# Performance work log

Hardware: AMD Instinct MI355X
Metric: run time of the kernel (lower is better)

The kernel has to match this reference:

```python
import jax, jax.numpy as jnp
import numpy as np

DIM = 256
HEADS = 8
DIM_FF = 1024
N = 4096
HEAD_DIM = DIM // HEADS
SCALE = HEAD_DIM ** -0.5


def layer_norm(x, gamma, beta, eps=1e-5):
    mu = jnp.mean(x, axis=-1, keepdims=True)
    var = jnp.var(x, axis=-1, keepdims=True)
    return (x - mu) * jax.lax.rsqrt(var + eps) * gamma + beta


def setup_inputs() -> dict:
    key = jax.random.key(0)
    ks = jax.random.split(key, 8)
    x = jax.random.normal(ks[0], (N, DIM), dtype=jnp.float32)
    adj = jax.random.randint(ks[1], (N, N), 0, 2, dtype=jnp.int32)
    adj = adj.at[jnp.arange(N), jnp.arange(N)].set(1)  # self-loops
    s = 1.0 / np.sqrt(DIM)
    w_qkv = jax.random.normal(ks[2], (DIM, 3 * DIM), dtype=jnp.float32) * s
    w_proj = jax.random.normal(ks[3], (DIM, DIM), dtype=jnp.float32) * s
    b_proj = jnp.zeros((DIM,), jnp.float32)
    w1 = jax.random.normal(ks[4], (DIM, DIM_FF), dtype=jnp.float32) * s
    b1 = jnp.zeros((DIM_FF,), jnp.float32)
    w2 = jax.random.normal(ks[5], (DIM_FF, DIM), dtype=jnp.float32) / np.sqrt(DIM_FF)
    b2 = jnp.zeros((DIM,), jnp.float32)
    g1 = jnp.ones((DIM,), jnp.float32)
    be1 = jnp.zeros((DIM,), jnp.float32)
    g2 = jnp.ones((DIM,), jnp.float32)
    be2 = jnp.zeros((DIM,), jnp.float32)
    return {"x": x, "adj": adj, "w_qkv": w_qkv, "w_proj": w_proj,
            "b_proj": b_proj, "w1": w1, "b1": b1, "w2": w2, "b2": b2,
            "g1": g1, "be1": be1, "g2": g2, "be2": be2}


def reference(x, adj, w_qkv, w_proj, b_proj, w1, b1, w2, b2, g1, be1, g2, be2):
    n = x.shape[0]
    qkv = layer_norm(x, g1, be1) @ w_qkv            # (N, 3*dim)
    qkv = qkv.reshape(n, 3, HEADS, HEAD_DIM)
    q, k, v = qkv[:, 0], qkv[:, 1], qkv[:, 2]       # (N, h, d)
    scores = jnp.einsum('nhd,mhd->hnm', q, k) * SCALE
    mask = (adj != 0)[None, :, :]                    # (1, N, N)
    scores = jnp.where(mask, scores, -jnp.inf)
    attn = jax.nn.softmax(scores, axis=-1)           # (h, N, N)
    out = jnp.einsum('hnm,mhd->nhd', attn, v).reshape(n, DIM)
    x = x + out @ w_proj + b_proj
    h2 = layer_norm(x, g2, be2)
    ff = jax.nn.gelu(h2 @ w1 + b1) @ w2 + b2
    return x + ff
```

## Files before the change

kernel.cpp:

```cpp
#include <hip/hip_runtime.h>
#include <hip/hip_bf16.h>

#define NT 4096
#define DM 256
#define NH 8
#define HD 32
#define DFF 1024

typedef __attribute__((ext_vector_type(8))) short s8v;
typedef __attribute__((ext_vector_type(4))) float f4v;
typedef __attribute__((ext_vector_type(2))) float f2v;
typedef __attribute__((ext_vector_type(16))) float f16v;
typedef __attribute__((ext_vector_type(4))) int i4v;

static __device__ __forceinline__ unsigned short f2b(float f){
  union{float f; unsigned u;} v; v.f=f;
  return (unsigned short)((v.u + 0x7FFFu + ((v.u>>16)&1u))>>16);
}

static __device__ __forceinline__ void gl_lds16(const void* g, void* l){
  __builtin_amdgcn_global_load_lds(
      (const __attribute__((address_space(1))) unsigned int*)g,
      (__attribute__((address_space(3))) unsigned int*)l, 16, 0, 0);
}

__global__ __launch_bounds__(256) void prologue_kernel(
    const int* __restrict__ adj, unsigned long long* __restrict__ mask,
    const float* __restrict__ wqkv, const float* __restrict__ wproj,
    const float* __restrict__ w1, const float* __restrict__ w2,
    unsigned short* __restrict__ wqkvT, unsigned short* __restrict__ wprojT,
    unsigned short* __restrict__ w1T, unsigned short* __restrict__ w2T,
    const float* __restrict__ x, const float* __restrict__ g1,
    const float* __restrict__ be1, unsigned short* __restrict__ h1){
  int bx = blockIdx.x;
  if (bx < 1024){
    int wv = threadIdx.x>>6, lane = threadIdx.x&63;
    int base = (bx*4 + wv)*64;
    for (int it=0; it<16; ++it){
      int w0 = base + it*4;
      unsigned long long b0 = __ballot(adj[(long)(w0+0)*64 + lane]!=0);
      unsigned long long b1 = __ballot(adj[(long)(w0+1)*64 + lane]!=0);
      unsigned long long b2 = __ballot(adj[(long)(w0+2)*64 + lane]!=0);
      unsigned long long b3 = __ballot(adj[(long)(w0+3)*64 + lane]!=0);
      if (lane==0){ mask[w0]=b0; mask[w0+1]=b1; mask[w0+2]=b2; mask[w0+3]=b3; }
    }
  } else if (bx < 1152){
    int t = (bx-1024)*256 + threadIdx.x;
    const int stride = 128*256;
    for (int i=t;i<768*DM;i+=stride){int n=i>>8,k=i&255; wqkvT[i]=f2b(wqkv[k*768+n]);}
    for (int i=t;i<DM*DM;i+=stride){int n=i>>8,k=i&255; wprojT[i]=f2b(wproj[k*DM+n]);}
    for (int i=t;i<DFF*DM;i+=stride){int n=i>>8,k=i&255; w1T[i]=f2b(w1[k*DFF+n]);}
    for (int i=t;i<DM*DFF;i+=stride){int n=i/DFF,k=i-n*DFF; w2T[i]=f2b(w2[k*DM+n]);}
  } else {
    int wv = threadIdx.x>>6, lane = threadIdx.x&63;
    int rbase = (bx-1152)*4 + wv;
    for (int j=0;j<8;j++){
      int row = rbase + j*512;
      float4 v = *(const float4*)(x + row*DM + lane*4);
      float s = v.x+v.y+v.z+v.w;
      float sq = v.x*v.x+v.y*v.y+v.z*v.z+v.w*v.w;
      #pragma unroll
      for (int m=1;m<64;m<<=1){ s += __shfl_xor(s,m); sq += __shfl_xor(sq,m); }
      float mu = s*(1.0f/DM);
      float rs = rsqrtf(sq*(1.0f/DM) - mu*mu + 1e-5f);
      float4 gv = *(const float4*)(g1 + lane*4);
      float4 bv = *(const float4*)(be1 + lane*4);
      ushort4 o;
      o.x = f2b((v.x-mu)*rs*gv.x + bv.x);
      o.y = f2b((v.y-mu)*rs*gv.y + bv.y);
      o.z = f2b((v.z-mu)*rs*gv.z + bv.z);
      o.w = f2b((v.w-mu)*rs*gv.w + bv.w);
      *(ushort4*)(h1 + row*DM + lane*4) = o;
    }
  }
}

template<int KD, int MODE>
__global__ __launch_bounds__(256,4) void gemm24(const unsigned short* __restrict__ A,
            const unsigned short* __restrict__ Wt, const float* __restrict__ bias,
            void* __restrict__ outp,
            unsigned short* __restrict__ Qp, unsigned short* __restrict__ Kp,
            unsigned short* __restrict__ Vt){
  int wv = threadIdx.x>>6, lane = threadIdx.x&63;
  int lo = lane&15, hi = lane>>4;
  int r0 = blockIdx.y*32;
  int cbase = blockIdx.x*256 + wv*16;
  const unsigned short* ar0 = A + (r0+lo)*KD + hi*8;
  const unsigned short* ar1 = ar0 + 16*KD;
  const unsigned short* br0 = Wt + (cbase     +lo)*KD + hi*8;
  const unsigned short* br1 = Wt + (cbase+ 64 +lo)*KD + hi*8;
  const unsigned short* br2 = Wt + (cbase+128 +lo)*KD + hi*8;
  const unsigned short* br3 = Wt + (cbase+192 +lo)*KD + hi*8;
  f4v c00={0,0,0,0},c01={0,0,0,0},c02={0,0,0,0},c03={0,0,0,0};
  f4v c10={0,0,0,0},c11={0,0,0,0},c12={0,0,0,0},c13={0,0,0,0};
  #pragma unroll 2
  for (int k0=0;k0<KD;k0+=32){
    s8v a0 = *(const s8v*)(ar0 + k0);
    s8v a1 = *(const s8v*)(ar1 + k0);
    s8v b0 = *(const s8v*)(br0 + k0);
    s8v b1 = *(const s8v*)(br1 + k0);
    s8v b2 = *(const s8v*)(br2 + k0);
    s8v b3 = *(const s8v*)(br3 + k0);
    c00 = __builtin_amdgcn_mfma_f32_16x16x32_bf16(a0,b0,c00,0,0,0);
    c10 = __builtin_amdgcn_mfma_f32_16x16x32_bf16(a1,b0,c10,0,0,0);
    c01 = __builtin_amdgcn_mfma_f32_16x16x32_bf16(a0,b1,c01,0,0,0);
    c11 = __builtin_amdgcn_mfma_f32_16x16x32_bf16(a1,b1,c11,0,0,0);
    c02 = __builtin_amdgcn_mfma_f32_16x16x32_bf16(a0,b2,c02,0,0,0);
    c12 = __builtin_amdgcn_mfma_f32_16x16x32_bf16(a1,b2,c12,0,0,0);
    c03 = __builtin_amdgcn_mfma_f32_16x16x32_bf16(a0,b3,c03,0,0,0);
    c13 = __builtin_amdgcn_mfma_f32_16x16x32_bf16(a1,b3,c13,0,0,0);
  }
  const float scl2 = (float)(0.17677669529663687 * 1.4426950408889634);
  #pragma unroll
  for (int rt=0;rt<2;rt++){
    f4v e0 = rt? c10:c00, e1 = rt? c11:c01, e2 = rt? c12:c02, e3 = rt? c13:c03;
    int nb = r0 + rt*16 + hi*4;
    #pragma unroll
    for (int jj=0;jj<4;jj++){
      f4v acc = jj==0?e0 : jj==1?e1 : jj==2?e2 : e3;
      int c = cbase + jj*64 + lo;
      if (MODE==0){
        int which = c>>8, hd = c&255, hh = hd>>5, d = hd&31;
        #pragma unroll
        for (int r=0;r<4;r++){
          int n = nb + r;
          float val = acc[r];
          if (which==0) Qp[(hh*NT+n)*HD+d]=f2b(val*scl2);
          else if (which==1) Kp[(hh*NT+n)*HD+d]=f2b(val);
          else Vt[(hh*HD+d)*NT+n]=f2b(val);
        }
      }
    }
  }
}

__global__ __launch_bounds__(512,2) void attn_kernel(
    const unsigned short* __restrict__ Q, const unsigned short* __restrict__ K,
    const unsigned short* __restrict__ Vt, const unsigned* __restrict__ mb32,
    unsigned short* __restrict__ out){
  __shared__ float Opart[8][32][34];
  __shared__ float llS[8][32];
  int wv = threadIdx.x>>6, lane = threadIdx.x&63;
  int l31 = lane&31, hi5 = lane>>5;
  int h = blockIdx.x, q0 = blockIdx.y*64;
  const unsigned short* QbA = Q + (h*NT + q0 + l31)*HD + hi5*8;
  const unsigned short* QbB = QbA + 32*HD;
  s8v bqA1 = *(const s8v*)(QbA);
  s8v bqA2 = *(const s8v*)(QbA + 16);
  s8v bqB1 = *(const s8v*)(QbB);
  s8v bqB2 = *(const s8v*)(QbB + 16);
  const unsigned short* Kb = K + h*NT*HD;
  const unsigned short* Vb = Vt + (h*HD + l31)*NT;
  const unsigned* mrowA = mb32 + (q0+l31)*(NT/32) + wv*16;
  const unsigned* mrowB = mrowA + 32*(NT/32);
  const float C0 = -11.541560327111707f;
  const f16v c0v = {C0,C0,C0,C0,C0,C0,C0,C0,C0,C0,C0,C0,C0,C0,C0,C0};
  f2v lacA = {0.f,0.f}, lacB = {0.f,0.f};
  f16v accA = {0,0,0,0,0,0,0,0,0,0,0,0,0,0,0,0};
  f16v accB = {0,0,0,0,0,0,0,0,0,0,0,0,0,0,0,0};
  union SU { f16v v; f2v p[8]; };
  const unsigned short* Kt0 = Kb + (wv*512 + l31)*HD + hi5*8;
  s8v kc1 = *(const s8v*)(Kt0);
  s8v kc2 = *(const s8v*)(Kt0 + 16);
  for (int tg=0; tg<4; tg++){
    i4v mw4A = *(const i4v*)(mrowA + tg*4);
    i4v mw4B = *(const i4v*)(mrowB + tg*4);
    #pragma unroll
    for (int ti=0; ti<4; ti++){
      int t = tg*4 + ti;
      int m0 = wv*512 + t*32;
      const unsigned short* Vtp = Vb + m0 + hi5*8;
      s8v av1 = *(const s8v*)(Vtp);
      s8v av2 = *(const s8v*)(Vtp + 16);
      int tn = (t<15)? t+1 : 15;
      const unsigned short* Ktn = Kb + (wv*512 + tn*32 + l31)*HD + hi5*8;
      s8v kn1 = *(const s8v*)(Ktn);
      s8v kn2 = *(const s8v*)(Ktn + 16);
      SU sa, sb;
      __builtin_amdgcn_s_setprio(1);
      sa.v = __builtin_amdgcn_mfma_f32_32x32x16_bf16(kc1, bqA1, c0v, 0,0,0);
      sa.v = __builtin_amdgcn_mfma_f32_32x32x16_bf16(kc2, bqA2, sa.v, 0,0,0);
      sb.v = __builtin_amdgcn_mfma_f32_32x32x16_bf16(kc1, bqB1, c0v, 0,0,0);
      sb.v = __builtin_amdgcn_mfma_f32_32x32x16_bf16(kc2, bqB2, sb.v, 0,0,0);
      __builtin_amdgcn_s_setprio(0);
      unsigned mwA = ((unsigned)mw4A[ti]) >> (4*hi5);
      unsigned mwB = ((unsigned)mw4B[ti]) >> (4*hi5);
      #pragma unroll
      for (int r=0;r<16;r++){
        int bp = (r&3)+8*(r>>2);
        float pa = __builtin_amdgcn_exp2f(sa.v[r]);
        float pb = __builtin_amdgcn_exp2f(sb.v[r]);
        sa.v[r] = ((mwA >> bp) & 1u) ? pa : 0.0f;
        sb.v[r] = ((mwB >> bp) & 1u) ? pb : 0.0f;
      }
      #pragma unroll
      for (int i=0;i<8;i++){ lacA += sa.p[i]; lacB += sb.p[i]; }
      unsigned a0,a1,a2,a3,a4,a5,a6,a7, b0,b1,b2,b3,b4,b5,b6,b7;
      asm("v_cvt_pk_bf16_f32 %0, %1, %2" : "=v"(a0) : "v"(sa.v[0]),  "v"(sa.v[1]));
      asm("v_cvt_pk_bf16_f32 %0, %1, %2" : "=v"(a1) : "v"(sa.v[2]),  "v"(sa.v[3]));
      asm("v_cvt_pk_bf16_f32 %0, %1, %2" : "=v"(a2) : "v"(sa.v[4]),  "v"(sa.v[5]));
      asm("v_cvt_pk_bf16_f32 %0, %1, %2" : "=v"(a3) : "v"(sa.v[6]),  "v"(sa.v[7]));
      asm("v_cvt_pk_bf16_f32 %0, %1, %2" : "=v"(a4) : "v"(sa.v[8]),  "v"(sa.v[9]));
      asm("v_cvt_pk_bf16_f32 %0, %1, %2" : "=v"(a5) : "v"(sa.v[10]), "v"(sa.v[11]));
      asm("v_cvt_pk_bf16_f32 %0, %1, %2" : "=v"(a6) : "v"(sa.v[12]), "v"(sa.v[13]));
      asm("v_cvt_pk_bf16_f32 %0, %1, %2" : "=v"(a7) : "v"(sa.v[14]), "v"(sa.v[15]));
      asm("v_permlane32_swap_b32 %0, %1" : "+v"(a0), "+v"(a2));
      asm("v_permlane32_swap_b32 %0, %1" : "+v"(a1), "+v"(a3));
      asm("v_permlane32_swap_b32 %0, %1" : "+v"(a4), "+v"(a6));
      asm("v_permlane32_swap_b32 %0, %1" : "+v"(a5), "+v"(a7));
      asm("v_cvt_pk_bf16_f32 %0, %1, %2" : "=v"(b0) : "v"(sb.v[0]),  "v"(sb.v[1]));
      asm("v_cvt_pk_bf16_f32 %0, %1, %2" : "=v"(b1) : "v"(sb.v[2]),  "v"(sb.v[3]));
      asm("v_cvt_pk_bf16_f32 %0, %1, %2" : "=v"(b2) : "v"(sb.v[4]),  "v"(sb.v[5]));
      asm("v_cvt_pk_bf16_f32 %0, %1, %2" : "=v"(b3) : "v"(sb.v[6]),  "v"(sb.v[7]));
      asm("v_cvt_pk_bf16_f32 %0, %1, %2" : "=v"(b4) : "v"(sb.v[8]),  "v"(sb.v[9]));
      asm("v_cvt_pk_bf16_f32 %0, %1, %2" : "=v"(b5) : "v"(sb.v[10]), "v"(sb.v[11]));
      asm("v_cvt_pk_bf16_f32 %0, %1, %2" : "=v"(b6) : "v"(sb.v[12]), "v"(sb.v[13]));
      asm("v_cvt_pk_bf16_f32 %0, %1, %2" : "=v"(b7) : "v"(sb.v[14]), "v"(sb.v[15]));
      asm("v_permlane32_swap_b32 %0, %1" : "+v"(b0), "+v"(b2));
      asm("v_permlane32_swap_b32 %0, %1" : "+v"(b1), "+v"(b3));
      asm("v_permlane32_swap_b32 %0, %1" : "+v"(b4), "+v"(b6));
      asm("v_permlane32_swap_b32 %0, %1" : "+v"(b5), "+v"(b7));
      i4v pA1i = {(int)a0,(int)a1,(int)a2,(int)a3};
      i4v pA2i = {(int)a4,(int)a5,(int)a6,(int)a7};
      i4v pB1i = {(int)b0,(int)b1,(int)b2,(int)b3};
      i4v pB2i = {(int)b4,(int)b5,(int)b6,(int)b7};
      s8v pA1 = __builtin_bit_cast(s8v, pA1i);
      s8v pA2 = __builtin_bit_cast(s8v, pA2i);
      s8v pB1 = __builtin_bit_cast(s8v, pB1i);
      s8v pB2 = __builtin_bit_cast(s8v, pB2i);
      __builtin_amdgcn_s_setprio(1);
      accA = __builtin_amdgcn_mfma_f32_32x32x16_bf16(av1, pA1, accA, 0,0,0);
      accA = __builtin_amdgcn_mfma_f32_32x32x16_bf16(av2, pA2, accA, 0,0,0);
      accB = __builtin_amdgcn_mfma_f32_32x32x16_bf16(av1, pB1, accB, 0,0,0);
      accB = __builtin_amdgcn_mfma_f32_32x32x16_bf16(av2, pB2, accB, 0,0,0);
      __builtin_amdgcn_s_setprio(0);
      kc1 = kn1; kc2 = kn2;
    }
  }
  int tid = threadIdx.x;
  int qq = tid>>4, dd = 2*(tid&15);
  #pragma unroll
  for (int i=0;i<8;i++){
    int d = (2*i&3) + 8*(i>>1) + 4*hi5;
    float2 p2; p2.x = accA[2*i]; p2.y = accA[2*i+1];
    *(float2*)&Opart[wv][l31][d] = p2;
  }
  float lsumA = lacA[0] + lacA[1];
  lsumA += __shfl_xor(lsumA, 32);
  if (hi5==0) llS[wv][l31] = lsumA;
  __syncthreads();
  {
    float L=0.f, o0=0.f, o1=0.f;
    #pragma unroll
    for (int u=0;u<8;u++){
      L  += llS[u][qq];
      o0 += Opart[u][qq][dd];
      o1 += Opart[u][qq][dd+1];
    }
    float inv = 1.0f/L;
    float r0 = o0*inv, r1 = o1*inv;
    unsigned pw;
    asm("v_cvt_pk_bf16_f32 %0, %1, %2" : "=v"(pw) : "v"(r0), "v"(r1));
    *(unsigned*)(out + (q0+qq)*DM + h*HD + dd) = pw;
  }
  __syncthreads();
  #pragma unroll
  for (int i=0;i<8;i++){
    int d = (2*i&3) + 8*(i>>1) + 4*hi5;
    float2 p2; p2.x = accB[2*i]; p2.y = accB[2*i+1];
    *(float2*)&Opart[wv][l31][d] = p2;
  }
  float lsumB = lacB[0] + lacB[1];
  lsumB += __shfl_xor(lsumB, 32);
  if (hi5==0) llS[wv][l31] = lsumB;
  __syncthreads();
  {
    float L=0.f, o0=0.f, o1=0.f;
    #pragma unroll
    for (int u=0;u<8;u++){
      L  += llS[u][qq];
      o0 += Opart[u][qq][dd];
      o1 += Opart[u][qq][dd+1];
    }
    float inv = 1.0f/L;
    float r0 = o0*inv, r1 = o1*inv;
    unsigned pw;
    asm("v_cvt_pk_bf16_f32 %0, %1, %2" : "=v"(pw) : "v"(r0), "v"(r1));
    *(unsigned*)(out + (q0+32+qq)*DM + h*HD + dd) = pw;
  }
}

__global__ __launch_bounds__(512,2) void tail_kernel(
    const unsigned short* __restrict__ ao, const unsigned short* __restrict__ wprojT,
    const float* __restrict__ bproj, const float* __restrict__ x,
    const float* __restrict__ g2, const float* __restrict__ be2,
    const unsigned short* __restrict__ w1T, const float* __restrict__ b1,
    const unsigned short* __restrict__ w2T, const float* __restrict__ b2,
    float* __restrict__ outp){
  __shared__ unsigned short h2L[16][DM];
  __shared__ unsigned short gL[16][DFF];
  __shared__ float Ss[8][16], Sq[8][16];
  __shared__ __align__(16) unsigned char w2S[2][32768];
  int wv = threadIdx.x>>6, lane = threadIdx.x&63;
  int lo = lane&15, hi = lane>>4;
  int tid = threadIdx.x;
  int r0 = blockIdx.x*16;
  float t[2][4];

#define STAGE_W2(KT, BUF)                                                     \
  { _Pragma("unroll")                                                         \
    for (int rr=0; rr<4; ++rr){                                               \
      int col_ = rr*64 + (tid>>3);                                            \
      int ko_  = (tid&7) ^ (col_&7);                                          \
      gl_lds16(w2T + col_*DFF + (KT)*64 + ko_*8,                              \
               &w2S[BUF][rr*8192 + tid*16]);                                  \
    } }

  {
    const unsigned short* ar  = ao + (r0+lo)*DM + hi*8;
    const unsigned short* pb0 = wprojT + (wv*16     +lo)*DM + hi*8;
    const unsigned short* pb1 = wprojT + (wv*16+128 +lo)*DM + hi*8;
    f4v a0={0,0,0,0}, a1={0,0,0,0};
    #pragma unroll
    for (int k0=0;k0<DM;k0+=32){
      s8v a = *(const s8v*)(ar + k0);
      a0 = __builtin_amdgcn_mfma_f32_16x16x32_bf16(a, *(const s8v*)(pb0+k0), a0,0,0,0);
      a1 = __builtin_amdgcn_mfma_f32_16x16x32_bf16(a, *(const s8v*)(pb1+k0), a1,0,0,0);
    }
    float sr[4]={0,0,0,0}, sq[4]={0,0,0,0};
    #pragma unroll
    for (int jj=0;jj<2;jj++){
      f4v acc = jj? a1 : a0;
      int c = jj*128 + wv*16 + lo;
      float bc = bproj[c];
      #pragma unroll
      for (int r=0;r<4;r++){
        int n = r0 + hi*4 + r;
        float tv = acc[r] + bc + x[n*DM+c];
        t[jj][r] = tv; sr[r] += tv; sq[r] += tv*tv;
      }
    }
    #pragma unroll
    for (int m=1;m<16;m<<=1){
      #pragma unroll
      for (int r=0;r<4;r++){ sr[r]+=__shfl_xor(sr[r],m); sq[r]+=__shfl_xor(sq[r],m); }
    }
    if (lo==0){
      #pragma unroll
      for (int r=0;r<4;r++){ Ss[wv][hi*4+r]=sr[r]; Sq[wv][hi*4+r]=sq[r]; }
    }
    __syncthreads();
    #pragma unroll
    for (int r=0;r<4;r++){
      int nl = hi*4+r;
      float S=0.f, Qs=0.f;
      #pragma unroll
      for (int u=0;u<8;u++){ S += Ss[u][nl]; Qs += Sq[u][nl]; }
      float mu = S*(1.0f/DM);
      float rs = rsqrtf(Qs*(1.0f/DM) - mu*mu + 1e-5f);
      #pragma unroll
      for (int jj=0;jj<2;jj++){
        int c = jj*128 + wv*16 + lo;
        unsigned short hv = f2b((t[jj][r]-mu)*rs*g2[c] + be2[c]);
        int g = c>>3;
        h2L[nl][((g^(nl&7))<<3) + (c&7)] = hv;
      }
    }
  }
  __syncthreads();

  STAGE_W2(0, 0);
  STAGE_W2(1, 1);

  #pragma unroll
  for (int p=0;p<2;p++){
    int cb = p*512 + wv*16;
    const unsigned short* wb0 = w1T + (cb      +lo)*DM + hi*8;
    const unsigned short* wb1 = w1T + (cb+128  +lo)*DM + hi*8;
    const unsigned short* wb2 = w1T + (cb+256  +lo)*DM + hi*8;
    const unsigned short* wb3 = w1T + (cb+384  +lo)*DM + hi*8;
    f4v c0={0,0,0,0},c1={0,0,0,0},c2={0,0,0,0},c3={0,0,0,0};
    #pragma unroll
    for (int k0=0;k0<DM;k0+=32){
      s8v a = *(const s8v*)&h2L[lo][(((hi + (k0>>3)) ^ (lo&7))<<3)];
      c0 = __builtin_amdgcn_mfma_f32_16x16x32_bf16(a, *(const s8v*)(wb0+k0), c0,0,0,0);
      c1 = __builtin_amdgcn_mfma_f32_16x16x32_bf16(a, *(const s8v*)(wb1+k0), c1,0,0,0);
      c2 = __builtin_amdgcn_mfma_f32_16x16x32_bf16(a, *(const s8v*)(wb2+k0), c2,0,0,0);
      c3 = __builtin_amdgcn_mfma_f32_16x16x32_bf16(a, *(const s8v*)(wb3+k0), c3,0,0,0);
    }
    #pragma unroll
    for (int jj=0;jj<4;jj++){
      f4v acc = jj==0?c0 : jj==1?c1 : jj==2?c2 : c3;
      int c = p*512 + jj*128 + wv*16 + lo;
      float bc = b1[c];
      #pragma unroll
      for (int r=0;r<4;r++){
        int nl = hi*4+r;
        float xx = acc[r] + bc;
        float x2v = xx*xx;
        float arg = xx*(2.302340531f + 0.102952640f*x2v);
        float e  = __builtin_amdgcn_exp2f(arg);
        float rcp = __builtin_amdgcn_rcpf(e + 1.0f);
        unsigned short gv = f2b(xx - xx*rcp);
        int g = c>>3;
        gL[nl][((g^(nl&7))<<3) + (c&7)] = gv;
      }
    }
  }
  __syncthreads();

  {
    f4v e0={0,0,0,0}, e1={0,0,0,0};
    int c0i = wv*16 + lo;
    int c1i = c0i + 128;
    for (int kt=0; kt<16; ++kt){
      if (kt>=1 && kt<15) STAGE_W2(kt+1, (kt+1)&1);
      const unsigned char* bufp = w2S[kt&1];
      #pragma unroll
      for (int ks=0; ks<2; ++ks){
        int k0 = kt*64 + ks*32;
        s8v a = *(const s8v*)&gL[lo][(((hi + (k0>>3)) ^ (lo&7))<<3)];
        s8v b0 = *(const s8v*)(bufp + c0i*128 + ((((ks*4)+hi) ^ (c0i&7))<<4));
        s8v b1 = *(const s8v*)(bufp + c1i*128 + ((((ks*4)+hi) ^ (c1i&7))<<4));
        e0 = __builtin_amdgcn_mfma_f32_16x16x32_bf16(a, b0, e0,0,0,0);
        e1 = __builtin_amdgcn_mfma_f32_16x16x32_bf16(a, b1, e1,0,0,0);
      }
      __syncthreads();
    }
    #pragma unroll
    for (int jj=0;jj<2;jj++){
      f4v acc = jj? e1 : e0;
      int c = jj*128 + wv*16 + lo;
      float bc = b2[c];
      #pragma unroll
      for (int r=0;r<4;r++){
        int n = r0 + hi*4 + r;
        outp[n*DM+c] = acc[r] + bc + t[jj][r];
      }
    }
  }
#undef STAGE_W2
}

extern "C" void kernel_launch(void* const* d_in, const int* in_sizes, int n_in,
                              void* d_out, int out_size, void* d_ws, size_t ws_size,
                              hipStream_t stream){
  const float* x     = (const float*)d_in[0];
  const int*   adj   = (const int*)d_in[1];
  const float* wqkv  = (const float*)d_in[2];
  const float* wproj = (const float*)d_in[3];
  const float* bproj = (const float*)d_in[4];
  const float* w1    = (const float*)d_in[5];
  const float* b1    = (const float*)d_in[6];
  const float* w2    = (const float*)d_in[7];
  const float* b2    = (const float*)d_in[8];
  const float* g1    = (const float*)d_in[9];
  const float* be1   = (const float*)d_in[10];
  const float* g2    = (const float*)d_in[11];
  const float* be2   = (const float*)d_in[12];

  char* ws = (char*)d_ws;
  unsigned short* h1    = (unsigned short*)(ws + (0u<<20));
  unsigned short* Qb    = (unsigned short*)(ws + (2u<<20));
  unsigned short* Kb    = (unsigned short*)(ws + (4u<<20));
  unsigned short* Vt    = (unsigned short*)(ws + (6u<<20));
  unsigned short* ao    = (unsigned short*)(ws + (8u<<20));
  unsigned short* wqkvT = (unsigned short*)(ws + (24u<<20));
  unsigned short* wprojT= (unsigned short*)(ws + (25u<<20));
  unsigned short* w1T   = (unsigned short*)(ws + (26u<<20));
  unsigned short* w2T   = (unsigned short*)(ws + (27u<<20));
  unsigned long long* mbits = (unsigned long long*)(ws + (28u<<20));
  float* outF = (float*)d_out;

  hipLaunchKernelGGL(prologue_kernel, dim3(1280), dim3(256), 0, stream,
                     adj, mbits, wqkv, wproj, w1, w2, wqkvT, wprojT, w1T, w2T,
                     x, g1, be1, h1);
  hipLaunchKernelGGL((gemm24<256,0>), dim3(3,128), dim3(256), 0, stream,
                     h1, wqkvT, nullptr, nullptr, Qb, Kb, Vt);
  hipLaunchKernelGGL(attn_kernel, dim3(8,64), dim3(512), 0, stream,
                     Qb, Kb, Vt, (const unsigned*)mbits, ao);
  hipLaunchKernelGGL(tail_kernel, dim3(256), dim3(512), 0, stream,
                     ao, wprojT, bproj, x, g2, be2, w1T, b1, w2T, b2, outF);
}
```

Baseline: 113.3 us.

## Stream W1 through double-buffered LDS via async global-to-LDS loads in tail kernel

The FF1 GEMM in the tail kernel used to read W1 straight from global memory into registers for the MFMAs. It now stages W1 in 64-wide k tiles into a shared double buffer using async global_load_lds, mirroring the existing W2 pipeline. The first two W1 stages are issued before the projection/LayerNorm phase so those loads overlap that work, and W2 staging starts at the end of the last W1 chunk. The cost is more __syncthreads barriers per block and a smaller per-wave N tile (2 accumulators instead of 4), which lowers MFMA ILP.

```diff
diff --git a/kernel.cpp b/kernel.cpp
--- a/kernel.cpp
+++ b/kernel.cpp
@@ -300,12 +300,22 @@
   __shared__ unsigned short h2L[16][DM];
   __shared__ unsigned short gL[16][DFF];
   __shared__ float Ss[8][16], Sq[8][16];
-  __shared__ __align__(16) unsigned char w2S[2][32768];
+  __shared__ __align__(16) unsigned char wS[2][32768];
   int wv = threadIdx.x>>6, lane = threadIdx.x&63;
   int lo = lane&15, hi = lane>>4;
   int tid = threadIdx.x;
   int r0 = blockIdx.x*16;
   float t[2][4];
+
+#define STAGE_W1(S_, BUF_)                                                    \
+  { int cb_ = (S_)>>2, kt_ = (S_)&3;                                          \
+    _Pragma("unroll")                                                         \
+    for (int rr=0; rr<4; ++rr){                                               \
+      int col_ = cb_*256 + rr*64 + (tid>>3);                                  \
+      int ko_  = (tid&7) ^ (col_&7);                                          \
+      gl_lds16(w1T + col_*DM + kt_*64 + ko_*8,                                \
+               &wS[BUF_][rr*8192 + tid*16]);                                  \
+    } }
 
 #define STAGE_W2(KT, BUF)                                                     \
   { _Pragma("unroll")                                                         \
@@ -313,8 +323,11 @@
       int col_ = rr*64 + (tid>>3);                                            \
       int ko_  = (tid&7) ^ (col_&7);                                          \
       gl_lds16(w2T + col_*DFF + (KT)*64 + ko_*8,                              \
-               &w2S[BUF][rr*8192 + tid*16]);                                  \
+               &wS[BUF][rr*8192 + tid*16]);                                   \
     } }
+
+  STAGE_W1(0, 0);
+  STAGE_W1(1, 1);
 
   {
     const unsigned short* ar  = ao + (r0+lo)*DM + hi*8;
@@ -369,29 +382,30 @@
   }
   __syncthreads();
 
-  STAGE_W2(0, 0);
-  STAGE_W2(1, 1);
-
-  #pragma unroll
-  for (int p=0;p<2;p++){
-    int cb = p*512 + wv*16;
-    const unsigned short* wb0 = w1T + (cb      +lo)*DM + hi*8;
-    const unsigned short* wb1 = w1T + (cb+128  +lo)*DM + hi*8;
-    const unsigned short* wb2 = w1T + (cb+256  +lo)*DM + hi*8;
-    const unsigned short* wb3 = w1T + (cb+384  +lo)*DM + hi*8;
-    f4v c0={0,0,0,0},c1={0,0,0,0},c2={0,0,0,0},c3={0,0,0,0};
-    #pragma unroll
-    for (int k0=0;k0<DM;k0+=32){
-      s8v a = *(const s8v*)&h2L[lo][(((hi + (k0>>3)) ^ (lo&7))<<3)];
-      c0 = __builtin_amdgcn_mfma_f32_16x16x32_bf16(a, *(const s8v*)(wb0+k0), c0,0,0,0);
-      c1 = __builtin_amdgcn_mfma_f32_16x16x32_bf16(a, *(const s8v*)(wb1+k0), c1,0,0,0);
-      c2 = __builtin_amdgcn_mfma_f32_16x16x32_bf16(a, *(const s8v*)(wb2+k0), c2,0,0,0);
-      c3 = __builtin_amdgcn_mfma_f32_16x16x32_bf16(a, *(const s8v*)(wb3+k0), c3,0,0,0);
-    }
-    #pragma unroll
-    for (int jj=0;jj<4;jj++){
-      f4v acc = jj==0?c0 : jj==1?c1 : jj==2?c2 : c3;
-      int c = p*512 + jj*128 + wv*16 + lo;
+  for (int cb=0; cb<4; ++cb){
+    f4v f0={0,0,0,0}, f1={0,0,0,0};
+    int c0i = wv*16 + lo;
+    int c1i = c0i + 128;
+    for (int kt=0; kt<4; ++kt){
+      int s = cb*4 + kt;
+      if (s>=1 && s<15) STAGE_W1(s+1, (s+1)&1);
+      const unsigned char* bufp = wS[s&1];
+      #pragma unroll
+      for (int ks=0; ks<2; ++ks){
+        int k0 = kt*64 + ks*32;
+        s8v a  = *(const s8v*)&h2L[lo][(((hi + (k0>>3)) ^ (lo&7))<<3)];
+        s8v bw0 = *(const s8v*)(bufp + c0i*128 + ((((ks*4)+hi) ^ (c0i&7))<<4));
+        s8v bw1 = *(const s8v*)(bufp + c1i*128 + ((((ks*4)+hi) ^ (c1i&7))<<4));
+        f0 = __builtin_amdgcn_mfma_f32_16x16x32_bf16(a, bw0, f0,0,0,0);
+        f1 = __builtin_amdgcn_mfma_f32_16x16x32_bf16(a, bw1, f1,0,0,0);
+      }
+      __syncthreads();
+    }
+    if (cb==3){ STAGE_W2(0, 0); STAGE_W2(1, 1); }
+    #pragma unroll
+    for (int jj=0;jj<2;jj++){
+      f4v acc = jj? f1 : f0;
+      int c = cb*256 + jj*128 + wv*16 + lo;
       float bc = b1[c];
       #pragma unroll
       for (int r=0;r<4;r++){
@@ -415,15 +429,15 @@
     int c1i = c0i + 128;
     for (int kt=0; kt<16; ++kt){
       if (kt>=1 && kt<15) STAGE_W2(kt+1, (kt+1)&1);
-      const unsigned char* bufp = w2S[kt&1];
+      const unsigned char* bufp = wS[kt&1];
       #pragma unroll
       for (int ks=0; ks<2; ++ks){
         int k0 = kt*64 + ks*32;
         s8v a = *(const s8v*)&gL[lo][(((hi + (k0>>3)) ^ (lo&7))<<3)];
-        s8v b0 = *(const s8v*)(bufp + c0i*128 + ((((ks*4)+hi) ^ (c0i&7))<<4));
-        s8v b1 = *(const s8v*)(bufp + c1i*128 + ((((ks*4)+hi) ^ (c1i&7))<<4));
-        e0 = __builtin_amdgcn_mfma_f32_16x16x32_bf16(a, b0, e0,0,0,0);
-        e1 = __builtin_amdgcn_mfma_f32_16x16x32_bf16(a, b1, e1,0,0,0);
+        s8v bw0 = *(const s8v*)(bufp + c0i*128 + ((((ks*4)+hi) ^ (c0i&7))<<4));
+        s8v bw1 = *(const s8v*)(bufp + c1i*128 + ((((ks*4)+hi) ^ (c1i&7))<<4));
+        e0 = __builtin_amdgcn_mfma_f32_16x16x32_bf16(a, bw0, e0,0,0,0);
+        e1 = __builtin_amdgcn_mfma_f32_16x16x32_bf16(a, bw1, e1,0,0,0);
       }
       __syncthreads();
     }
@@ -439,6 +453,7 @@
       }
     }
   }
+#undef STAGE_W1
 #undef STAGE_W2
 }
 
```

New measurement: 111.4 us. No clear change (-1.7%).
